# Performance work log

Measured on AMD Instinct MI355X. Metric: run time of the kernel, lower is better.

Reference implementation:

```python
import jax, jax.numpy as jnp
import numpy as np

N = 20000   # nodes per graph
E = 320000  # edges per graph
D_IN, D_H = 128, 304


def _param(key, shape, fan_in):
    return jax.random.normal(key, shape, dtype=jnp.float32) / np.sqrt(fan_in)


def setup_inputs() -> dict:
    key = jax.random.key(0)
    ks = jax.random.split(key, 20)
    inp = {}
    for i, name in enumerate(['x1', 'x2', 'x3']):
        inp[name] = jax.random.normal(ks[i], (N, D_IN), dtype=jnp.float32)
    for i, name in enumerate(['src1', 'dst1', 'src2', 'dst2', 'src3', 'dst3']):
        inp[name] = jax.random.randint(ks[3 + i], (E,), 0, N, dtype=jnp.int32)
    # shared GraphConv weights (DGL GraphConv: h = norm_agg(x) @ W + b)
    inp['W1'] = _param(ks[9], (D_IN, D_H), D_IN)
    inp['b1'] = jnp.zeros((D_H,), jnp.float32)
    inp['W2'] = _param(ks[10], (D_H, D_H), D_H)
    inp['b2'] = jnp.zeros((D_H,), jnp.float32)
    inp['W3'] = _param(ks[11], (D_H, D_H), D_H)
    inp['b3'] = jnp.zeros((D_H,), jnp.float32)
    # MLP head: 304 -> 128 -> 64 -> 1
    inp['fW1'] = _param(ks[12], (D_H, 128), D_H)
    inp['fb1'] = jnp.zeros((128,), jnp.float32)
    inp['fW2'] = _param(ks[13], (128, 64), 128)
    inp['fb2'] = jnp.zeros((64,), jnp.float32)
    inp['fW3'] = _param(ks[14], (64, 1), 64)
    inp['fb3'] = jnp.zeros((1,), jnp.float32)
    return inp


def gcn_conv(x, src, dst, W, b):
    # DGL GraphConv, norm='both': h = D_in^{-1/2} A D_out^{-1/2} x W + b
    ones = jnp.ones((src.shape[0],), x.dtype)
    out_deg = jnp.clip(jax.ops.segment_sum(ones, src, num_segments=N), 1.0)
    in_deg = jnp.clip(jax.ops.segment_sum(ones, dst, num_segments=N), 1.0)
    h = x * jax.lax.rsqrt(out_deg)[:, None]
    agg = jax.ops.segment_sum(h[src], dst, num_segments=N)  # [N, d] SpMM
    agg = agg * jax.lax.rsqrt(in_deg)[:, None]
    return agg @ W + b


def reference(x1, x2, x3, src1, dst1, src2, dst2, src3, dst3,
              W1, b1, W2, b2, W3, b3, fW1, fb1, fW2, fb2, fW3, fb3):
    def branch(x, src, dst):
        x = jax.nn.relu(gcn_conv(x, src, dst, W1, b1))
        x = jax.nn.relu(gcn_conv(x, src, dst, W2, b2))
        x = jax.nn.relu(gcn_conv(x, src, dst, W3, b3))
        return x

    h1 = branch(x1, src1, dst1)
    h2 = branch(x2, src2, dst2)
    h3 = branch(x3, src3, dst3)
    # multi_graph_opt='max': max over all nodes of all three graphs -> [304]
    pooled = jnp.max(jnp.concatenate([h1, h2, h3], axis=0), axis=0)
    # output_opt='fc': MLP head with sigmoid
    z = jax.nn.relu(pooled @ fW1 + fb1)
    z = jax.nn.relu(z @ fW2 + fb2)
    return jax.nn.sigmoid(z @ fW3 + fb3)  # shape [1]
```

## Files before the change

### kernel.cpp

```cpp
#include <hip/hip_runtime.h>
#include <hip/hip_bf16.h>
#include <math.h>

#define NODES 20000
#define EDGES 320000
#define NB 3
#define TOTN (NODES * NB)
#define TOTE (EDGES * NB)
#define D_IN 128
#define D_H 304
#define SCAN_B 59
#define SLICES 40
#define SLICE_E (EDGES / SLICES)
#define ZX TOTN
#define ZQ (TOTN + 96)

typedef __attribute__((ext_vector_type(4))) float f32x4;
typedef __attribute__((ext_vector_type(2))) float f32x2;

__device__ __forceinline__ unsigned short f2bf(float f) {
    unsigned u = __float_as_uint(f);
    unsigned r = (u + 0x7fffu + ((u >> 16) & 1u)) >> 16;
    return (unsigned short)r;
}
__device__ __forceinline__ void gload16(const void* g, void* l) {
    __builtin_amdgcn_global_load_lds(
        (const __attribute__((address_space(1))) unsigned*)g,
        (__attribute__((address_space(3))) unsigned*)l, 16, 0, 0);
}

__global__ void k_pack8(const float4* __restrict__ x1, const float4* __restrict__ x2,
                        const float4* __restrict__ x3, const float* __restrict__ inv_out,
                        unsigned* __restrict__ q) {
    const int per = NODES * D_IN / 4;
    int i = blockIdx.x * 256 + threadIdx.x;
    if (i >= 3 * per) return;
    const float4* s; int j;
    if (i < per)          { s = x1; j = i; }
    else if (i < 2 * per) { s = x2; j = i - per; }
    else                  { s = x3; j = i - 2 * per; }
    float4 v = s[j];
    float sc = inv_out[i >> 5];
    int p = __builtin_amdgcn_cvt_pk_fp8_f32(v.x * sc, v.y * sc, 0, false);
    p = __builtin_amdgcn_cvt_pk_fp8_f32(v.z * sc, v.w * sc, p, true);
    q[i] = (unsigned)p;
}

__global__ __launch_bounds__(256, 1) void k_hist(
    const int* __restrict__ s1, const int* __restrict__ d1,
    const int* __restrict__ s2, const int* __restrict__ d2,
    const int* __restrict__ s3, const int* __restrict__ d3,
    int* __restrict__ partial_in, int* __restrict__ partial_out) {
    __shared__ int hist[NODES];
    int g = blockIdx.x / SLICES, s = blockIdx.x % SLICES;
    bool isOut = (blockIdx.y == 1);
    const int* ep;
    if (isOut) ep = (g == 0) ? s1 : ((g == 1) ? s2 : s3);
    else       ep = (g == 0) ? d1 : ((g == 1) ? d2 : d3);
    ep += s * SLICE_E;
    for (int i = threadIdx.x; i < NODES; i += 256) hist[i] = 0;
    __syncthreads();
    const int4* ep4 = (const int4*)ep;
    for (int i = threadIdx.x; i < SLICE_E / 4; i += 256) {
        int4 v = ep4[i];
        atomicAdd(&hist[v.x], 1);
        atomicAdd(&hist[v.y], 1);
        atomicAdd(&hist[v.z], 1);
        atomicAdd(&hist[v.w], 1);
    }
    __syncthreads();
    int* po = (isOut ? partial_out : partial_in) + (size_t)blockIdx.x * NODES;
    for (int i = threadIdx.x; i < NODES; i += 256) po[i] = hist[i];
}

__global__ void k_degscan(const int* __restrict__ partial_in,
                          const int* __restrict__ partial_out,
                          float* __restrict__ inv_in, float* __restrict__ inv_out,
                          int* __restrict__ excl, int* __restrict__ btot) {
    __shared__ int wsum[16];
    int b = blockIdx.x, t = threadIdx.x;
    int i = b * 1024 + t;
    int lane = t & 63, wid = t >> 6;
    int v = 0;
    if (i < TOTN) {
        int g = i / NODES, ln = i - g * NODES;
        const int* pi = partial_in + (size_t)g * SLICES * NODES + ln;
        const int* po = partial_out + (size_t)g * SLICES * NODES + ln;
        int ci = 0, co = 0;
        #pragma unroll
        for (int s = 0; s < SLICES; s++) { ci += pi[s * NODES]; co += po[s * NODES]; }
        v = ci;
        inv_in[i]  = 1.0f / sqrtf((float)max(ci, 1));
        inv_out[i] = 1.0f / sqrtf((float)max(co, 1));
    }
    int sv = v;
    #pragma unroll
    for (int o = 1; o < 64; o <<= 1) {
        int u = __shfl_up(sv, o, 64);
        if (lane >= o) sv += u;
    }
    if (lane == 63) wsum[wid] = sv;
    __syncthreads();
    if (t < 16) {
        int w = wsum[t];
        #pragma unroll
        for (int o = 1; o < 16; o <<= 1) {
            int u = __shfl_up(w, o, 16);
            if (t >= o) w += u;
        }
        wsum[t] = w;
    }
    __syncthreads();
    int wbase = (wid > 0) ? wsum[wid - 1] : 0;
    if (i < TOTN) excl[i] = wbase + sv - v;
    if (t == 0) btot[b] = wsum[15];
}

__global__ void k_scanB(const int* __restrict__ btot, int* __restrict__ boff,
                        int* __restrict__ csr_slack, int* __restrict__ pooled,
                        unsigned* __restrict__ x8z, unsigned* __restrict__ q8z) {
    int t = threadIdx.x;
    if (t < 32) csr_slack[t] = 0;
    if (t < 32) x8z[t] = 0;
    #pragma unroll
    for (int i = t; i < 80; i += 64) q8z[i] = 0;
    #pragma unroll
    for (int i = t; i < 320; i += 64) pooled[i] = 0;
    int v = (t < SCAN_B) ? btot[t] : 0;
    int sv = v;
    #pragma unroll
    for (int o = 1; o < 64; o <<= 1) {
        int u = __shfl_up(sv, o, 64);
        if (t >= o) sv += u;
    }
    if (t < SCAN_B) boff[t] = sv - v;
}

__global__ void k_offC(const int* __restrict__ excl, const int* __restrict__ boff,
                       const int* __restrict__ partial_in,
                       int* __restrict__ row_ptr, int* __restrict__ O) {
    int n = blockIdx.x * 256 + threadIdx.x;
    if (n >= TOTN) {
        if (n == TOTN) row_ptr[TOTN] = TOTE;
        return;
    }
    if (n == 0) row_ptr[TOTN] = TOTE;
    int rp = excl[n] + boff[n >> 10];
    row_ptr[n] = rp;
    int g = n / NODES, ln = n - g * NODES;
    const int* pi = partial_in + (size_t)g * SLICES * NODES + ln;
    int* on = O + (size_t)g * SLICES * NODES + ln;
    int run = rp;
    #pragma unroll
    for (int s = 0; s < SLICES; s++) {
        on[s * NODES] = run;
        run += pi[s * NODES];
    }
}

__global__ __launch_bounds__(256, 1) void k_fill2(
    const int* __restrict__ s1, const int* __restrict__ d1,
    const int* __restrict__ s2, const int* __restrict__ d2,
    const int* __restrict__ s3, const int* __restrict__ d3,
    const int* __restrict__ O, int* __restrict__ csr) {
    __shared__ int cur[NODES];
    int g = blockIdx.x / SLICES, s = blockIdx.x % SLICES;
    const int* sp = (g == 0) ? s1 : ((g == 1) ? s2 : s3);
    const int* dp = (g == 0) ? d1 : ((g == 1) ? d2 : d3);
    sp += s * SLICE_E; dp += s * SLICE_E;
    const int* on = O + (size_t)blockIdx.x * NODES;
    for (int i = threadIdx.x; i < NODES; i += 256) cur[i] = on[i];
    __syncthreads();
    int base = g * NODES;
    const int4* sp4 = (const int4*)sp;
    const int4* dp4 = (const int4*)dp;
    for (int i = threadIdx.x; i < SLICE_E / 4; i += 256) {
        int4 dv = dp4[i];
        int4 sv = sp4[i];
        int p0 = atomicAdd(&cur[dv.x], 1); csr[p0] = sv.x + base;
        int p1 = atomicAdd(&cur[dv.y], 1); csr[p1] = sv.y + base;
        int p2 = atomicAdd(&cur[dv.z], 1); csr[p2] = sv.z + base;
        int p3 = atomicAdd(&cur[dv.w], 1); csr[p3] = sv.w + base;
    }
}

__global__ void k_spmm_l1(const uint2* __restrict__ h, unsigned char* __restrict__ agg,
                          const int* __restrict__ row_ptr, const int* __restrict__ csr,
                          const float* __restrict__ inv_in) {
    int n = blockIdx.x * 4 + (threadIdx.x >> 6);
    int lane = threadIdx.x & 63;
    int s = lane >> 4;
    int off = lane & 15;
    f32x2 a[4];
    #pragma unroll
    for (int j = 0; j < 4; j++) a[j] = (f32x2){0.f, 0.f};
    int k0 = row_ptr[n], k1 = row_ptr[n + 1];
    const int* cp = csr + k0 + s;
    int e[8];
    #pragma unroll
    for (int j = 0; j < 8; j++) {
        int ev = cp[4 * j];
        e[j] = (k0 + s + 4 * j < k1) ? ev : ZX;
    }
    uint2 u[8];
    #pragma unroll
    for (int j = 0; j < 8; j++) u[j] = h[(size_t)e[j] * 16 + off];
    #pragma unroll
    for (int j = 0; j < 8; j++) {
        a[0] += __builtin_amdgcn_cvt_pk_f32_fp8(u[j].x, false);
        a[1] += __builtin_amdgcn_cvt_pk_f32_fp8(u[j].x, true);
        a[2] += __builtin_amdgcn_cvt_pk_f32_fp8(u[j].y, false);
        a[3] += __builtin_amdgcn_cvt_pk_f32_fp8(u[j].y, true);
    }
    for (int k = k0 + 32 + s; k < k1; k += 4) {
        int e0 = csr[k];
        uint2 u0 = h[(size_t)e0 * 16 + off];
        a[0] += __builtin_amdgcn_cvt_pk_f32_fp8(u0.x, false);
        a[1] += __builtin_amdgcn_cvt_pk_f32_fp8(u0.x, true);
        a[2] += __builtin_amdgcn_cvt_pk_f32_fp8(u0.y, false);
        a[3] += __builtin_amdgcn_cvt_pk_f32_fp8(u0.y, true);
    }
    float r[8];
    #pragma unroll
    for (int j = 0; j < 4; j++) {
        #pragma unroll
        for (int c = 0; c < 2; c++) {
            float v = a[j][c];
            r[2 * j + c] = v + __shfl(v, lane + 16, 64)
                             + __shfl(v, lane + 32, 64)
                             + __shfl(v, lane + 48, 64);
        }
    }
    if (lane < 16) {
        float wi = inv_in[n];
        int d0 = __builtin_amdgcn_cvt_pk_fp8_f32(r[0] * wi, r[1] * wi, 0, false);
        d0 = __builtin_amdgcn_cvt_pk_fp8_f32(r[2] * wi, r[3] * wi, d0, true);
        int d1 = __builtin_amdgcn_cvt_pk_fp8_f32(r[4] * wi, r[5] * wi, 0, false);
        d1 = __builtin_amdgcn_cvt_pk_fp8_f32(r[6] * wi, r[7] * wi, d1, true);
        uint2 st; st.x = (unsigned)d0; st.y = (unsigned)d1;
        *(uint2*)(agg + (size_t)n * 128 + lane * 8) = st;
    }
}

__global__ void k_spmm_big(const uint4* __restrict__ h, unsigned char* __restrict__ agg,
                           const int* __restrict__ row_ptr, const int* __restrict__ csr,
                           const float* __restrict__ inv_in) {
    int n = blockIdx.x * 4 + (threadIdx.x >> 6);
    int lane = threadIdx.x & 63;
    int s = lane / 20;
    int off = lane % 20;
    f32x2 a[8];
    #pragma unroll
    for (int j = 0; j < 8; j++) a[j] = (f32x2){0.f, 0.f};
    int k0 = row_ptr[n], k1 = row_ptr[n + 1];
    int k1g = (s < 3) ? k1 : k0;
    const int* cp = csr + k0 + s;
    int e[8];
    #pragma unroll
    for (int j = 0; j < 8; j++) {
        int ev = cp[3 * j];
        e[j] = (k0 + s + 3 * j < k1g) ? ev : ZQ;
    }
    uint4 u[8];
    #pragma unroll
    for (int j = 0; j < 8; j++) u[j] = h[(size_t)e[j] * 20 + off];
    #pragma unroll
    for (int j = 0; j < 8; j++) {
        a[0] += __builtin_amdgcn_cvt_pk_f32_fp8(u[j].x, false);
        a[1] += __builtin_amdgcn_cvt_pk_f32_fp8(u[j].x, true);
        a[2] += __builtin_amdgcn_cvt_pk_f32_fp8(u[j].y, false);
        a[3] += __builtin_amdgcn_cvt_pk_f32_fp8(u[j].y, true);
        a[4] += __builtin_amdgcn_cvt_pk_f32_fp8(u[j].z, false);
        a[5] += __builtin_amdgcn_cvt_pk_f32_fp8(u[j].z, true);
        a[6] += __builtin_amdgcn_cvt_pk_f32_fp8(u[j].w, false);
        a[7] += __builtin_amdgcn_cvt_pk_f32_fp8(u[j].w, true);
    }
    for (int k = k0 + 24 + s; k < k1g; k += 3) {
        int e0 = csr[k];
        uint4 u0 = h[(size_t)e0 * 20 + off];
        a[0] += __builtin_amdgcn_cvt_pk_f32_fp8(u0.x, false);
        a[1] += __builtin_amdgcn_cvt_pk_f32_fp8(u0.x, true);
        a[2] += __builtin_amdgcn_cvt_pk_f32_fp8(u0.y, false);
        a[3] += __builtin_amdgcn_cvt_pk_f32_fp8(u0.y, true);
        a[4] += __builtin_amdgcn_cvt_pk_f32_fp8(u0.z, false);
        a[5] += __builtin_amdgcn_cvt_pk_f32_fp8(u0.z, true);
        a[6] += __builtin_amdgcn_cvt_pk_f32_fp8(u0.w, false);
        a[7] += __builtin_amdgcn_cvt_pk_f32_fp8(u0.w, true);
    }
    float r[16];
    #pragma unroll
    for (int j = 0; j < 8; j++) {
        #pragma unroll
        for (int c = 0; c < 2; c++) {
            float v = a[j][c];
            r[2 * j + c] = v + __shfl(v, lane + 20, 64) + __shfl(v, lane + 40, 64);
        }
    }
    if (lane < 20) {
        float wi = inv_in[n];
        int d0 = __builtin_amdgcn_cvt_pk_fp8_f32(r[0] * wi, r[1] * wi, 0, false);
        d0 = __builtin_amdgcn_cvt_pk_fp8_f32(r[2] * wi, r[3] * wi, d0, true);
        int d1 = __builtin_amdgcn_cvt_pk_fp8_f32(r[4] * wi, r[5] * wi, 0, false);
        d1 = __builtin_amdgcn_cvt_pk_fp8_f32(r[6] * wi, r[7] * wi, d1, true);
        int d2 = __builtin_amdgcn_cvt_pk_fp8_f32(r[8] * wi, r[9] * wi, 0, false);
        d2 = __builtin_amdgcn_cvt_pk_fp8_f32(r[10] * wi, r[11] * wi, d2, true);
        int d3 = __builtin_amdgcn_cvt_pk_fp8_f32(r[12] * wi, r[13] * wi, 0, false);
        d3 = __builtin_amdgcn_cvt_pk_fp8_f32(r[14] * wi, r[15] * wi, d3, true);
        uint4 st; st.x = (unsigned)d0; st.y = (unsigned)d1; st.z = (unsigned)d2; st.w = (unsigned)d3;
        *(uint4*)(agg + (size_t)n * 320 + lane * 16) = st;
    }
}

__global__ void k_prepw_all(const float* __restrict__ W1, const float* __restrict__ W2,
                            const float* __restrict__ W3,
                            unsigned char* __restrict__ Wt1, unsigned char* __restrict__ Wt2,
                            unsigned char* __restrict__ Wt3) {
    const int N1 = D_H * 128, N2 = D_H * 320;
    int id = blockIdx.x * 256 + threadIdx.x;
    const float* W; unsigned char* Wt; int K, Kpad, lid;
    if (id < N1)                { W = W1; Wt = Wt1; K = 128; Kpad = 128; lid = id; }
    else if (id < N1 + N2)      { W = W2; Wt = Wt2; K = 304; Kpad = 320; lid = id - N1; }
    else if (id < N1 + 2 * N2)  { W = W3; Wt = Wt3; K = 304; Kpad = 320; lid = id - N1 - N2; }
    else return;
    int n = lid / Kpad, k = lid - n * Kpad;
    unsigned char v = 0;
    if (k < K) {
        float w = W[k * D_H + n];
        v = (unsigned char)(__builtin_amdgcn_cvt_pk_fp8_f32(w, w, 0, false) & 0xff);
    }
    Wt[lid] = v;
}

template <int MODE>
__global__ __launch_bounds__(256, 2) void k_gemm_mfma(
    const unsigned char* __restrict__ A, int lda,
    const unsigned char* __restrict__ Wt,
    const float* __restrict__ bias,
    const float* __restrict__ inv_out,
    unsigned char* __restrict__ C8, int* __restrict__ gpool, int M, int K) {
    __shared__ char SM[40960];
    __shared__ int pmax[D_H];
    char* As = SM;
    char* Bs = SM + 8192;
    int tid = threadIdx.x;
    int wv = tid >> 6, lane = tid & 63;
    int quad = lane >> 4, lrow = lane & 15;
    int bm = blockIdx.x * 128;

    if (MODE == 1) {
        for (int i = tid; i < D_H; i += 256) pmax[i] = 0;
    }

    f32x4 acc[2][19];
    #pragma unroll
    for (int r = 0; r < 2; r++)
        #pragma unroll
        for (int t = 0; t < 19; t++) acc[r][t] = (f32x4){0.f, 0.f, 0.f, 0.f};

    int swz = (lrow & 3) ^ (lrow >> 2);
    int hb = (quad & 1) * 8;

    for (int kt = 0; kt < K; kt += 64) {
        #pragma unroll
        for (int j = 0; j < 2; j++) {
            int c = j * 256 + tid;
            int row = c >> 2, xc = c & 3;
            int col = xc ^ (row & 3) ^ ((row >> 2) & 3);
            gload16(A + (size_t)(bm + row) * lda + kt + col * 16, As + c * 16);
        }
        #pragma unroll
        for (int j = 0; j < 5; j++) {
            int c = j * 256 + tid;
            if (c < 1216) {
                int row = c >> 2, xc = c & 3;
                int col = xc ^ (row & 3) ^ ((row >> 2) & 3);
                gload16(Wt + (size_t)row * K + kt + col * 16, Bs + c * 16);
            }
        }
        __syncthreads();
        #pragma unroll
        for (int sub = 0; sub < 2; sub++) {
            int c0 = sub * 2 + (quad >> 1);
            int cx = (c0 ^ swz) * 16 + hb;
            int ra = wv * 32 + lrow;
            long long a0 = *(const long long*)(As + ra * 64 + cx);
            long long a1 = *(const long long*)(As + (ra + 16) * 64 + cx);
            #pragma unroll
            for (int t = 0; t < 19; t++) {
                long long b = *(const long long*)(Bs + (t * 16 + lrow) * 64 + cx);
                acc[0][t] = __builtin_amdgcn_mfma_f32_16x16x32_fp8_fp8(a0, b, acc[0][t], 0, 0, 0);
                acc[1][t] = __builtin_amdgcn_mfma_f32_16x16x32_fp8_fp8(a1, b, acc[1][t], 0, 0, 0);
            }
        }
        __syncthreads();
    }
    if (MODE == 0) {
        unsigned char* OUT = (unsigned char*)SM;
        if (tid < 128) *(uint4*)(OUT + tid * 320 + 304) = make_uint4(0u, 0u, 0u, 0u);
        #pragma unroll
        for (int t = 0; t < 19; t++) {
            int col = t * 16 + lrow;
            float bv = bias[col];
            #pragma unroll
            for (int r = 0; r < 2; r++) {
                int rl = wv * 32 + r * 16 + quad * 4;
                #pragma unroll
                for (int g = 0; g < 4; g++) {
                    int row = bm + rl + g;
                    float sc = inv_out[min(row, M - 1)];
                    float v = fmaxf(acc[r][t][g] + bv, 0.f) * sc;
                    int p = __builtin_amdgcn_cvt_pk_fp8_f32(v, v, 0, false);
                    OUT[(rl + g) * 320 + col] = (unsigned char)(p & 0xff);
                }
            }
        }
        __syncthreads();
        #pragma unroll
        for (int j = 0; j < 10; j++) {
            int c = j * 256 + tid;
            *(uint4*)(C8 + (size_t)bm * 320 + (size_t)c * 16) = *(const uint4*)(OUT + c * 16);
        }
    } else {
        #pragma unroll
        for (int t = 0; t < 19; t++) {
            int col = t * 16 + lrow;
            float bv = bias[col];
            float m = 0.f;
            #pragma unroll
            for (int r = 0; r < 2; r++) {
                int rbase = bm + wv * 32 + r * 16 + quad * 4;
                #pragma unroll
                for (int g = 0; g < 4; g++) {
                    int row = rbase + g;
                    if (row < M) m = fmaxf(m, fmaxf(acc[r][t][g] + bv, 0.f));
                }
            }
            atomicMax(&pmax[col], __float_as_int(m));
        }
        __syncthreads();
        for (int i = tid; i < D_H; i += 256)
            atomicMax(&gpool[i], pmax[i]);
    }
}

__global__ void k_mlp(const int* __restrict__ pooled_i,
                      const float* __restrict__ fW1, const float* __restrict__ fb1,
                      const float* __restrict__ fW2, const float* __restrict__ fb2,
                      const float* __restrict__ fW3, const float* __restrict__ fb3,
                      float* __restrict__ out) {
    __shared__ float p[D_H];
    __shared__ float z1[128];
    __shared__ float z2[64];
    int t = threadIdx.x;
    if (t < D_H) p[t] = __int_as_float(pooled_i[t]);
    __syncthreads();
    if (t < 128) {
        float acc = fb1[t];
        for (int k = 0; k < D_H; k++) acc += p[k] * fW1[k * 128 + t];
        z1[t] = fmaxf(acc, 0.f);
    }
    __syncthreads();
    if (t < 64) {
        float acc = fb2[t];
        for (int k = 0; k < 128; k++) acc += z1[k] * fW2[k * 64 + t];
        z2[t] = fmaxf(acc, 0.f);
    }
    __syncthreads();
    if (t == 0) {
        float acc = fb3[0];
        for (int k = 0; k < 64; k++) acc += z2[k] * fW3[k];
        out[0] = 1.f / (1.f + expf(-acc));
    }
}

extern "C" void kernel_launch(void* const* d_in, const int* in_sizes, int n_in,
                              void* d_out, int out_size, void* d_ws, size_t ws_size,
                              hipStream_t stream) {
    const float* x1 = (const float*)d_in[0];
    const float* x2 = (const float*)d_in[1];
    const float* x3 = (const float*)d_in[2];
    const int* src1 = (const int*)d_in[3];
    const int* dst1 = (const int*)d_in[4];
    const int* src2 = (const int*)d_in[5];
    const int* dst2 = (const int*)d_in[6];
    const int* src3 = (const int*)d_in[7];
    const int* dst3 = (const int*)d_in[8];
    const float* W1 = (const float*)d_in[9];
    const float* b1 = (const float*)d_in[10];
    const float* W2 = (const float*)d_in[11];
    const float* b2 = (const float*)d_in[12];
    const float* W3 = (const float*)d_in[13];
    const float* b3 = (const float*)d_in[14];
    const float* fW1 = (const float*)d_in[15];
    const float* fb1 = (const float*)d_in[16];
    const float* fW2 = (const float*)d_in[17];
    const float* fb2 = (const float*)d_in[18];
    const float* fW3 = (const float*)d_in[19];
    const float* fb3 = (const float*)d_in[20];
    float* out = (float*)d_out;

    char* w = (char*)d_ws;
    unsigned* X8       = (unsigned*)w;      w += (size_t)(TOTN + 1) * 32 * 4;
    unsigned char* Q8  = (unsigned char*)w; w += (size_t)(TOTN + 128) * 320;
    unsigned char* P8  = (unsigned char*)w; w += (size_t)(TOTN + 128) * 320;
    unsigned char* Wt1 = (unsigned char*)w; w += (size_t)D_H * 128;
    unsigned char* Wt2 = (unsigned char*)w; w += (size_t)D_H * 320;
    unsigned char* Wt3 = (unsigned char*)w; w += (size_t)D_H * 320;
    w = (char*)(((size_t)w + 255) & ~(size_t)255);
    int* partial_in  = (int*)w;  w += (size_t)NB * SLICES * NODES * 4;
    int* partial_out = (int*)w;  w += (size_t)NB * SLICES * NODES * 4;
    int* O           = (int*)w;  w += (size_t)NB * SLICES * NODES * 4;
    float* inv_out = (float*)w;  w += (size_t)TOTN * 4;
    float* inv_in  = (float*)w;  w += (size_t)TOTN * 4;
    int* row_ptr   = (int*)w;    w += (size_t)(TOTN + 4) * 4;
    int* csr       = (int*)w;    w += (size_t)(TOTE + 32) * 4;
    int* excl      = (int*)w;    w += (size_t)TOTN * 4;
    int* btot      = (int*)w;    w += 64 * 4;
    int* boff      = (int*)w;    w += 64 * 4;
    int* pooled    = (int*)w;    w += 320 * 4;

    k_hist<<<dim3(NB * SLICES, 2), 256, 0, stream>>>(src1, dst1, src2, dst2, src3, dst3,
                                                     partial_in, partial_out);
    k_degscan<<<SCAN_B, 1024, 0, stream>>>(partial_in, partial_out,
                                           inv_in, inv_out, excl, btot);
    k_pack8<<<(3 * NODES * D_IN / 4 + 255) / 256, 256, 0, stream>>>(
        (const float4*)x1, (const float4*)x2, (const float4*)x3, inv_out, X8);
    k_scanB<<<1, 64, 0, stream>>>(btot, boff, csr + TOTE, pooled,
                                  X8 + (size_t)ZX * 32,
                                  (unsigned*)(Q8 + (size_t)ZQ * 320));
    k_offC<<<(TOTN + 256) / 256, 256, 0, stream>>>(excl, boff, partial_in, row_ptr, O);
    k_fill2<<<NB * SLICES, 256, 0, stream>>>(src1, dst1, src2, dst2, src3, dst3, O, csr);
    k_prepw_all<<<(D_H * (128 + 320 + 320) + 255) / 256, 256, 0, stream>>>(
        W1, W2, W3, Wt1, Wt2, Wt3);

    int ggrid = (TOTN + 127) / 128;

    k_spmm_l1<<<TOTN / 4, 256, 0, stream>>>((const uint2*)X8, P8, row_ptr, csr, inv_in);
    k_gemm_mfma<0><<<ggrid, 256, 0, stream>>>(P8, 128, Wt1, b1, inv_out,
                                              Q8, nullptr, TOTN, 128);
    k_spmm_big<<<TOTN / 4, 256, 0, stream>>>((const uint4*)Q8, P8, row_ptr, csr, inv_in);
    k_gemm_mfma<0><<<ggrid, 256, 0, stream>>>(P8, 320, Wt2, b2, inv_out,
                                              Q8, nullptr, TOTN, 320);
    k_spmm_big<<<TOTN / 4, 256, 0, stream>>>((const uint4*)Q8, P8, row_ptr, csr, inv_in);
    k_gemm_mfma<1><<<ggrid, 256, 0, stream>>>(P8, 320, Wt3, b3, nullptr,
                                              nullptr, pooled, TOTN, 320);

    k_mlp<<<1, 320, 0, stream>>>(pooled, fW1, fb1, fW2, fb2, fW3, fb3, out);
}
```

Measured before the change: 342.6 us.

## Merge preprocessing kernels and use atomic-based scan with row-end pointers

Fuses input packing with weight conversion into one launch, replaces the two-pass block scan with a global atomic counter that assigns each block's CSR offset, and folds buffer zeroing into the offset kernel, removing several small launches. Partial degree histograms are stored as 16-bit values to cut traffic. Row ranges become start/end arrays, so CSR segments may be placed in non-monotonic order, and the SpMM prologue skips loads for rows with few edges. The atomic ordering is nondeterministic but stays correct as long as each row's start and end are used together.

```diff
diff --git a/kernel.cpp b/kernel.cpp
--- a/kernel.cpp
+++ b/kernel.cpp
@@ -14,44 +14,62 @@
 #define SLICE_E (EDGES / SLICES)
 #define ZX TOTN
 #define ZQ (TOTN + 96)
+#define PACKB 7500
 
 typedef __attribute__((ext_vector_type(4))) float f32x4;
 typedef __attribute__((ext_vector_type(2))) float f32x2;
 
-__device__ __forceinline__ unsigned short f2bf(float f) {
-    unsigned u = __float_as_uint(f);
-    unsigned r = (u + 0x7fffu + ((u >> 16) & 1u)) >> 16;
-    return (unsigned short)r;
-}
 __device__ __forceinline__ void gload16(const void* g, void* l) {
     __builtin_amdgcn_global_load_lds(
         (const __attribute__((address_space(1))) unsigned*)g,
         (__attribute__((address_space(3))) unsigned*)l, 16, 0, 0);
 }
 
-__global__ void k_pack8(const float4* __restrict__ x1, const float4* __restrict__ x2,
-                        const float4* __restrict__ x3, const float* __restrict__ inv_out,
-                        unsigned* __restrict__ q) {
-    const int per = NODES * D_IN / 4;
-    int i = blockIdx.x * 256 + threadIdx.x;
-    if (i >= 3 * per) return;
-    const float4* s; int j;
-    if (i < per)          { s = x1; j = i; }
-    else if (i < 2 * per) { s = x2; j = i - per; }
-    else                  { s = x3; j = i - 2 * per; }
-    float4 v = s[j];
-    float sc = inv_out[i >> 5];
-    int p = __builtin_amdgcn_cvt_pk_fp8_f32(v.x * sc, v.y * sc, 0, false);
-    p = __builtin_amdgcn_cvt_pk_fp8_f32(v.z * sc, v.w * sc, p, true);
-    q[i] = (unsigned)p;
+__global__ void k_pack_prepw(const float4* __restrict__ x1, const float4* __restrict__ x2,
+                             const float4* __restrict__ x3, const float* __restrict__ inv_out,
+                             unsigned* __restrict__ q,
+                             const float* __restrict__ W1, const float* __restrict__ W2,
+                             const float* __restrict__ W3,
+                             unsigned char* __restrict__ Wt1, unsigned char* __restrict__ Wt2,
+                             unsigned char* __restrict__ Wt3) {
+    if (blockIdx.x < PACKB) {
+        const int per = NODES * D_IN / 4;
+        int i = blockIdx.x * 256 + threadIdx.x;
+        const float4* s; int j;
+        if (i < per)          { s = x1; j = i; }
+        else if (i < 2 * per) { s = x2; j = i - per; }
+        else                  { s = x3; j = i - 2 * per; }
+        float4 v = s[j];
+        float sc = inv_out[i >> 5];
+        int p = __builtin_amdgcn_cvt_pk_fp8_f32(v.x * sc, v.y * sc, 0, false);
+        p = __builtin_amdgcn_cvt_pk_fp8_f32(v.z * sc, v.w * sc, p, true);
+        q[i] = (unsigned)p;
+    } else {
+        const int N1 = D_H * 128, N2 = D_H * 320;
+        int id = (blockIdx.x - PACKB) * 256 + threadIdx.x;
+        const float* W; unsigned char* Wt; int K, Kpad, lid;
+        if (id < N1)                { W = W1; Wt = Wt1; K = 128; Kpad = 128; lid = id; }
+        else if (id < N1 + N2)      { W = W2; Wt = Wt2; K = 304; Kpad = 320; lid = id - N1; }
+        else if (id < N1 + 2 * N2)  { W = W3; Wt = Wt3; K = 304; Kpad = 320; lid = id - N1 - N2; }
+        else return;
+        int n = lid / Kpad, k = lid - n * Kpad;
+        unsigned char v = 0;
+        if (k < K) {
+            float w = W[k * D_H + n];
+            v = (unsigned char)(__builtin_amdgcn_cvt_pk_fp8_f32(w, w, 0, false) & 0xff);
+        }
+        Wt[lid] = v;
+    }
 }
 
 __global__ __launch_bounds__(256, 1) void k_hist(
     const int* __restrict__ s1, const int* __restrict__ d1,
     const int* __restrict__ s2, const int* __restrict__ d2,
     const int* __restrict__ s3, const int* __restrict__ d3,
-    int* __restrict__ partial_in, int* __restrict__ partial_out) {
+    unsigned short* __restrict__ partial_in, unsigned short* __restrict__ partial_out,
+    int* __restrict__ gctr) {
     __shared__ int hist[NODES];
+    if (blockIdx.x == 0 && blockIdx.y == 0 && threadIdx.x == 0) *gctr = 0;
     int g = blockIdx.x / SLICES, s = blockIdx.x % SLICES;
     bool isOut = (blockIdx.y == 1);
     const int* ep;
@@ -69,23 +87,25 @@
         atomicAdd(&hist[v.w], 1);
     }
     __syncthreads();
-    int* po = (isOut ? partial_out : partial_in) + (size_t)blockIdx.x * NODES;
-    for (int i = threadIdx.x; i < NODES; i += 256) po[i] = hist[i];
-}
-
-__global__ void k_degscan(const int* __restrict__ partial_in,
-                          const int* __restrict__ partial_out,
+    unsigned short* po = (isOut ? partial_out : partial_in) + (size_t)blockIdx.x * NODES;
+    for (int i = threadIdx.x; i < NODES; i += 256) po[i] = (unsigned short)hist[i];
+}
+
+__global__ void k_degscan(const unsigned short* __restrict__ partial_in,
+                          const unsigned short* __restrict__ partial_out,
                           float* __restrict__ inv_in, float* __restrict__ inv_out,
-                          int* __restrict__ excl, int* __restrict__ btot) {
+                          int* __restrict__ row_ptr, int* __restrict__ rend,
+                          int* __restrict__ gctr) {
     __shared__ int wsum[16];
+    __shared__ int sbase;
     int b = blockIdx.x, t = threadIdx.x;
     int i = b * 1024 + t;
     int lane = t & 63, wid = t >> 6;
     int v = 0;
     if (i < TOTN) {
         int g = i / NODES, ln = i - g * NODES;
-        const int* pi = partial_in + (size_t)g * SLICES * NODES + ln;
-        const int* po = partial_out + (size_t)g * SLICES * NODES + ln;
+        const unsigned short* pi = partial_in + (size_t)g * SLICES * NODES + ln;
+        const unsigned short* po = partial_out + (size_t)g * SLICES * NODES + ln;
         int ci = 0, co = 0;
         #pragma unroll
         for (int s = 0; s < SLICES; s++) { ci += pi[s * NODES]; co += po[s * NODES]; }
@@ -111,44 +131,33 @@
         wsum[t] = w;
     }
     __syncthreads();
+    if (t == 0) sbase = atomicAdd(gctr, wsum[15]);
+    __syncthreads();
     int wbase = (wid > 0) ? wsum[wid - 1] : 0;
-    if (i < TOTN) excl[i] = wbase + sv - v;
-    if (t == 0) btot[b] = wsum[15];
-}
-
-__global__ void k_scanB(const int* __restrict__ btot, int* __restrict__ boff,
-                        int* __restrict__ csr_slack, int* __restrict__ pooled,
-                        unsigned* __restrict__ x8z, unsigned* __restrict__ q8z) {
-    int t = threadIdx.x;
-    if (t < 32) csr_slack[t] = 0;
-    if (t < 32) x8z[t] = 0;
-    #pragma unroll
-    for (int i = t; i < 80; i += 64) q8z[i] = 0;
-    #pragma unroll
-    for (int i = t; i < 320; i += 64) pooled[i] = 0;
-    int v = (t < SCAN_B) ? btot[t] : 0;
-    int sv = v;
-    #pragma unroll
-    for (int o = 1; o < 64; o <<= 1) {
-        int u = __shfl_up(sv, o, 64);
-        if (t >= o) sv += u;
-    }
-    if (t < SCAN_B) boff[t] = sv - v;
-}
-
-__global__ void k_offC(const int* __restrict__ excl, const int* __restrict__ boff,
-                       const int* __restrict__ partial_in,
-                       int* __restrict__ row_ptr, int* __restrict__ O) {
+    if (i < TOTN) {
+        int rp = sbase + wbase + sv - v;
+        row_ptr[i] = rp;
+        rend[i] = rp + v;
+    }
+}
+
+__global__ void k_offC(const int* __restrict__ row_ptr,
+                       const unsigned short* __restrict__ partial_in,
+                       int* __restrict__ O,
+                       int* __restrict__ csr_slack, unsigned* __restrict__ x8z,
+                       unsigned* __restrict__ q8z, int* __restrict__ pooled) {
     int n = blockIdx.x * 256 + threadIdx.x;
     if (n >= TOTN) {
-        if (n == TOTN) row_ptr[TOTN] = TOTE;
+        int ex = n - TOTN;
+        if (ex < 32) csr_slack[ex] = 0;
+        else if (ex < 64) x8z[ex - 32] = 0;
+        else if (ex < 144) q8z[ex - 64] = 0;
+        else if (ex < 464) pooled[ex - 144] = 0;
         return;
     }
-    if (n == 0) row_ptr[TOTN] = TOTE;
-    int rp = excl[n] + boff[n >> 10];
-    row_ptr[n] = rp;
+    int rp = row_ptr[n];
     int g = n / NODES, ln = n - g * NODES;
-    const int* pi = partial_in + (size_t)g * SLICES * NODES + ln;
+    const unsigned short* pi = partial_in + (size_t)g * SLICES * NODES + ln;
     int* on = O + (size_t)g * SLICES * NODES + ln;
     int run = rp;
     #pragma unroll
@@ -185,7 +194,8 @@
 }
 
 __global__ void k_spmm_l1(const uint2* __restrict__ h, unsigned char* __restrict__ agg,
-                          const int* __restrict__ row_ptr, const int* __restrict__ csr,
+                          const int* __restrict__ row_ptr, const int* __restrict__ rend,
+                          const int* __restrict__ csr,
                           const float* __restrict__ inv_in) {
     int n = blockIdx.x * 4 + (threadIdx.x >> 6);
     int lane = threadIdx.x & 63;
@@ -194,23 +204,27 @@
     f32x2 a[4];
     #pragma unroll
     for (int j = 0; j < 4; j++) a[j] = (f32x2){0.f, 0.f};
-    int k0 = row_ptr[n], k1 = row_ptr[n + 1];
+    int k0 = row_ptr[n], k1 = rend[n];
+    int deg = k1 - k0;
     const int* cp = csr + k0 + s;
     int e[8];
     #pragma unroll
     for (int j = 0; j < 8; j++) {
         int ev = cp[4 * j];
-        e[j] = (k0 + s + 4 * j < k1) ? ev : ZX;
+        e[j] = (s + 4 * j < deg) ? ev : ZX;
     }
     uint2 u[8];
     #pragma unroll
-    for (int j = 0; j < 8; j++) u[j] = h[(size_t)e[j] * 16 + off];
+    for (int j = 0; j < 8; j++)
+        if (4 * j < deg) u[j] = h[(size_t)e[j] * 16 + off];
     #pragma unroll
     for (int j = 0; j < 8; j++) {
-        a[0] += __builtin_amdgcn_cvt_pk_f32_fp8(u[j].x, false);
-        a[1] += __builtin_amdgcn_cvt_pk_f32_fp8(u[j].x, true);
-        a[2] += __builtin_amdgcn_cvt_pk_f32_fp8(u[j].y, false);
-        a[3] += __builtin_amdgcn_cvt_pk_f32_fp8(u[j].y, true);
+        if (4 * j < deg) {
+            a[0] += __builtin_amdgcn_cvt_pk_f32_fp8(u[j].x, false);
+            a[1] += __builtin_amdgcn_cvt_pk_f32_fp8(u[j].x, true);
+            a[2] += __builtin_amdgcn_cvt_pk_f32_fp8(u[j].y, false);
+            a[3] += __builtin_amdgcn_cvt_pk_f32_fp8(u[j].y, true);
+        }
     }
     for (int k = k0 + 32 + s; k < k1; k += 4) {
         int e0 = csr[k];
@@ -243,7 +257,8 @@
 }
 
 __global__ void k_spmm_big(const uint4* __restrict__ h, unsigned char* __restrict__ agg,
-                           const int* __restrict__ row_ptr, const int* __restrict__ csr,
+                           const int* __restrict__ row_ptr, const int* __restrict__ rend,
+                           const int* __restrict__ csr,
                            const float* __restrict__ inv_in) {
     int n = blockIdx.x * 4 + (threadIdx.x >> 6);
     int lane = threadIdx.x & 63;
@@ -252,29 +267,34 @@
     f32x2 a[8];
     #pragma unroll
     for (int j = 0; j < 8; j++) a[j] = (f32x2){0.f, 0.f};
-    int k0 = row_ptr[n], k1 = row_ptr[n + 1];
-    int k1g = (s < 3) ? k1 : k0;
+    int k0 = row_ptr[n], k1 = rend[n];
+    int deg = k1 - k0;
+    int degg = (s < 3) ? deg : 0;
     const int* cp = csr + k0 + s;
     int e[8];
     #pragma unroll
     for (int j = 0; j < 8; j++) {
         int ev = cp[3 * j];
-        e[j] = (k0 + s + 3 * j < k1g) ? ev : ZQ;
+        e[j] = (s + 3 * j < degg) ? ev : ZQ;
     }
     uint4 u[8];
     #pragma unroll
-    for (int j = 0; j < 8; j++) u[j] = h[(size_t)e[j] * 20 + off];
+    for (int j = 0; j < 8; j++)
+        if (3 * j < deg) u[j] = h[(size_t)e[j] * 20 + off];
     #pragma unroll
     for (int j = 0; j < 8; j++) {
-        a[0] += __builtin_amdgcn_cvt_pk_f32_fp8(u[j].x, false);
-        a[1] += __builtin_amdgcn_cvt_pk_f32_fp8(u[j].x, true);
-        a[2] += __builtin_amdgcn_cvt_pk_f32_fp8(u[j].y, false);
-        a[3] += __builtin_amdgcn_cvt_pk_f32_fp8(u[j].y, true);
-        a[4] += __builtin_amdgcn_cvt_pk_f32_fp8(u[j].z, false);
-        a[5] += __builtin_amdgcn_cvt_pk_f32_fp8(u[j].z, true);
-        a[6] += __builtin_amdgcn_cvt_pk_f32_fp8(u[j].w, false);
-        a[7] += __builtin_amdgcn_cvt_pk_f32_fp8(u[j].w, true);
-    }
+        if (3 * j < deg) {
+            a[0] += __builtin_amdgcn_cvt_pk_f32_fp8(u[j].x, false);
+            a[1] += __builtin_amdgcn_cvt_pk_f32_fp8(u[j].x, true);
+            a[2] += __builtin_amdgcn_cvt_pk_f32_fp8(u[j].y, false);
+            a[3] += __builtin_amdgcn_cvt_pk_f32_fp8(u[j].y, true);
+            a[4] += __builtin_amdgcn_cvt_pk_f32_fp8(u[j].z, false);
+            a[5] += __builtin_amdgcn_cvt_pk_f32_fp8(u[j].z, true);
+            a[6] += __builtin_amdgcn_cvt_pk_f32_fp8(u[j].w, false);
+            a[7] += __builtin_amdgcn_cvt_pk_f32_fp8(u[j].w, true);
+        }
+    }
+    int k1g = k0 + degg;
     for (int k = k0 + 24 + s; k < k1g; k += 3) {
         int e0 = csr[k];
         uint4 u0 = h[(size_t)e0 * 20 + off];
@@ -309,26 +329,6 @@
         uint4 st; st.x = (unsigned)d0; st.y = (unsigned)d1; st.z = (unsigned)d2; st.w = (unsigned)d3;
         *(uint4*)(agg + (size_t)n * 320 + lane * 16) = st;
     }
-}
-
-__global__ void k_prepw_all(const float* __restrict__ W1, const float* __restrict__ W2,
-                            const float* __restrict__ W3,
-                            unsigned char* __restrict__ Wt1, unsigned char* __restrict__ Wt2,
-                            unsigned char* __restrict__ Wt3) {
-    const int N1 = D_H * 128, N2 = D_H * 320;
-    int id = blockIdx.x * 256 + threadIdx.x;
-    const float* W; unsigned char* Wt; int K, Kpad, lid;
-    if (id < N1)                { W = W1; Wt = Wt1; K = 128; Kpad = 128; lid = id; }
-    else if (id < N1 + N2)      { W = W2; Wt = Wt2; K = 304; Kpad = 320; lid = id - N1; }
-    else if (id < N1 + 2 * N2)  { W = W3; Wt = Wt3; K = 304; Kpad = 320; lid = id - N1 - N2; }
-    else return;
-    int n = lid / Kpad, k = lid - n * Kpad;
-    unsigned char v = 0;
-    if (k < K) {
-        float w = W[k * D_H + n];
-        v = (unsigned char)(__builtin_amdgcn_cvt_pk_fp8_f32(w, w, 0, false) & 0xff);
-    }
-    Wt[lid] = v;
 }
 
 template <int MODE>
@@ -507,41 +507,38 @@
     unsigned char* Wt2 = (unsigned char*)w; w += (size_t)D_H * 320;
     unsigned char* Wt3 = (unsigned char*)w; w += (size_t)D_H * 320;
     w = (char*)(((size_t)w + 255) & ~(size_t)255);
-    int* partial_in  = (int*)w;  w += (size_t)NB * SLICES * NODES * 4;
-    int* partial_out = (int*)w;  w += (size_t)NB * SLICES * NODES * 4;
-    int* O           = (int*)w;  w += (size_t)NB * SLICES * NODES * 4;
+    unsigned short* partial_in  = (unsigned short*)w; w += (size_t)NB * SLICES * NODES * 2;
+    unsigned short* partial_out = (unsigned short*)w; w += (size_t)NB * SLICES * NODES * 2;
+    int* O         = (int*)w;    w += (size_t)NB * SLICES * NODES * 4;
     float* inv_out = (float*)w;  w += (size_t)TOTN * 4;
     float* inv_in  = (float*)w;  w += (size_t)TOTN * 4;
-    int* row_ptr   = (int*)w;    w += (size_t)(TOTN + 4) * 4;
+    int* row_ptr   = (int*)w;    w += (size_t)TOTN * 4;
+    int* rend      = (int*)w;    w += (size_t)TOTN * 4;
     int* csr       = (int*)w;    w += (size_t)(TOTE + 32) * 4;
-    int* excl      = (int*)w;    w += (size_t)TOTN * 4;
-    int* btot      = (int*)w;    w += 64 * 4;
-    int* boff      = (int*)w;    w += 64 * 4;
     int* pooled    = (int*)w;    w += 320 * 4;
+    int* gctr      = (int*)w;    w += 64;
 
     k_hist<<<dim3(NB * SLICES, 2), 256, 0, stream>>>(src1, dst1, src2, dst2, src3, dst3,
-                                                     partial_in, partial_out);
+                                                     partial_in, partial_out, gctr);
     k_degscan<<<SCAN_B, 1024, 0, stream>>>(partial_in, partial_out,
-                                           inv_in, inv_out, excl, btot);
-    k_pack8<<<(3 * NODES * D_IN / 4 + 255) / 256, 256, 0, stream>>>(
-        (const float4*)x1, (const float4*)x2, (const float4*)x3, inv_out, X8);
-    k_scanB<<<1, 64, 0, stream>>>(btot, boff, csr + TOTE, pooled,
-                                  X8 + (size_t)ZX * 32,
-                                  (unsigned*)(Q8 + (size_t)ZQ * 320));
-    k_offC<<<(TOTN + 256) / 256, 256, 0, stream>>>(excl, boff, partial_in, row_ptr, O);
+                                           inv_in, inv_out, row_ptr, rend, gctr);
+    k_pack_prepw<<<PACKB + 912, 256, 0, stream>>>(
+        (const float4*)x1, (const float4*)x2, (const float4*)x3, inv_out, X8,
+        W1, W2, W3, Wt1, Wt2, Wt3);
+    k_offC<<<(TOTN + 464 + 255) / 256, 256, 0, stream>>>(
+        row_ptr, partial_in, O, csr + TOTE,
+        X8 + (size_t)ZX * 32, (unsigned*)(Q8 + (size_t)ZQ * 320), pooled);
     k_fill2<<<NB * SLICES, 256, 0, stream>>>(src1, dst1, src2, dst2, src3, dst3, O, csr);
-    k_prepw_all<<<(D_H * (128 + 320 + 320) + 255) / 256, 256, 0, stream>>>(
-        W1, W2, W3, Wt1, Wt2, Wt3);
 
     int ggrid = (TOTN + 127) / 128;
 
-    k_spmm_l1<<<TOTN / 4, 256, 0, stream>>>((const uint2*)X8, P8, row_ptr, csr, inv_in);
+    k_spmm_l1<<<TOTN / 4, 256, 0, stream>>>((const uint2*)X8, P8, row_ptr, rend, csr, inv_in);
     k_gemm_mfma<0><<<ggrid, 256, 0, stream>>>(P8, 128, Wt1, b1, inv_out,
                                               Q8, nullptr, TOTN, 128);
-    k_spmm_big<<<TOTN / 4, 256, 0, stream>>>((const uint4*)Q8, P8, row_ptr, csr, inv_in);
+    k_spmm_big<<<TOTN / 4, 256, 0, stream>>>((const uint4*)Q8, P8, row_ptr, rend, csr, inv_in);
     k_gemm_mfma<0><<<ggrid, 256, 0, stream>>>(P8, 320, Wt2, b2, inv_out,
                                               Q8, nullptr, TOTN, 320);
-    k_spmm_big<<<TOTN / 4, 256, 0, stream>>>((const uint4*)Q8, P8, row_ptr, csr, inv_in);
+    k_spmm_big<<<TOTN / 4, 256, 0, stream>>>((const uint4*)Q8, P8, row_ptr, rend, csr, inv_in);
     k_gemm_mfma<1><<<ggrid, 256, 0, stream>>>(P8, 320, Wt3, b3, nullptr,
                                               nullptr, pooled, TOTN, 320);
 
```

New measurement: 327.2 us. 4.5% less time.
